# Performance work log

Measured on AMD Instinct MI355X. Metric: run time of the kernel, lower is better.

The kernel has to match this reference:

```python
import jax, jax.numpy as jnp
import numpy as np

NUM_HEADS = 8
DIM_KEY = 64
WINDOW = 16
TEMP = float(np.power(DIM_KEY, 0.5))


def setup_inputs() -> dict:
    key = jax.random.key(0)
    k1, k2, k3, k4 = jax.random.split(key, 4)
    B, T, H = 4, 2048, 512
    std = np.sqrt(2.0 / (H + DIM_KEY))
    return {
        "query": jax.random.normal(k1, (B, T, H), dtype=jnp.float32),
        "key": jax.random.normal(k2, (B, T, H), dtype=jnp.float32),
        "Wq": jax.random.normal(k3, (NUM_HEADS * DIM_KEY, H), dtype=jnp.float32) * std,
        "bq": jnp.zeros((NUM_HEADS * DIM_KEY,), dtype=jnp.float32),
        "Wk": jax.random.normal(k4, (NUM_HEADS * DIM_KEY, H), dtype=jnp.float32) * std,
        "bk": jnp.zeros((NUM_HEADS * DIM_KEY,), dtype=jnp.float32),
    }


def reference(query, key, Wq, bq, Wk, bk):
    B, T, _ = query.shape
    w = WINDOW
    # linear projections, split into heads: [B, T, H, dk]
    q = (jnp.einsum("bti,oi->bto", query, Wq) + bq).reshape(B, T, NUM_HEADS, DIM_KEY)
    k = (jnp.einsum("bti,oi->bto", key, Wk) + bk).reshape(B, T, NUM_HEADS, DIM_KEY)
    # dense scores [B, H, Tq, Tk]
    attn = jnp.einsum("bqhd,bkhd->bhqk", q, k) / TEMP
    # window mask (get_window_mask): allowed where i-w <= j <= i+w
    i = jnp.arange(T)[:, None]
    j = jnp.arange(T)[None, :]
    allowed = (j >= i - w) & (j <= i + w)  # [T, T]
    attn = jnp.where(allowed[None, None], attn, -jnp.inf)
    attn = jax.nn.softmax(attn, axis=-1)
    # select mask gather (get_select_mask): each row keeps 2w+1 cols
    # starting at clip(i - w, 0, T - (2w+1))
    starts = jnp.clip(jnp.arange(T) - w, 0, T - (2 * w + 1))  # [T]
    idx = starts[:, None] + jnp.arange(2 * w + 1)[None, :]  # [T, 2w+1]
    out = jnp.take_along_axis(attn, idx[None, None, :, :], axis=-1)
    return out  # [B, NUM_HEADS, T, 2w+1]
```

## Files before the change

### kernel.cpp

```cpp
#include <hip/hip_runtime.h>
#include <hip/hip_bf16.h>
#include <math.h>

#define TT 2048
#define HH 512
#define NH 8
#define DK 64
#define WIN 16
#define NC 33

typedef __attribute__((ext_vector_type(8))) short bf16x8;
typedef __attribute__((ext_vector_type(4))) float f32x4;

__device__ inline ushort f2bf(float f) {
  uint u = __builtin_bit_cast(uint, f);
  return (ushort)((u + 0x7FFFu + ((u >> 16) & 1u)) >> 16);
}
__device__ inline ushort cvt1(float f) {
  __hip_bfloat16 h = __float2bfloat16(f);
  return __builtin_bit_cast(ushort, h);
}

__global__ __launch_bounds__(256) void cvt_w(
    const float* __restrict__ Wq, const float* __restrict__ Wk,
    ushort* __restrict__ Wqb, ushort* __restrict__ Wkb)
{
  const int id = blockIdx.x * 256 + threadIdx.x;
  const float* src = (id < 32768) ? Wq : Wk;
  ushort* dst = (id < 32768) ? Wqb : Wkb;
  const int off = (id & 32767) * 8;
  float4 x = *(const float4*)(src + off);
  float4 y = *(const float4*)(src + off + 4);
  union { ushort s[8]; uint4 v; } pk;
  pk.s[0]=cvt1(x.x); pk.s[1]=cvt1(x.y); pk.s[2]=cvt1(x.z); pk.s[3]=cvt1(x.w);
  pk.s[4]=cvt1(y.x); pk.s[5]=cvt1(y.y); pk.s[6]=cvt1(y.z); pk.s[7]=cvt1(y.w);
  *(uint4*)(dst + off) = pk.v;
}

#define PBM 128
#define PBN 128
#define PBK 64

__global__ __launch_bounds__(256) void proj_mfma(
    const float* __restrict__ Aq, const float* __restrict__ Ak,
    const ushort* __restrict__ Wqb, const ushort* __restrict__ Wkb,
    const float* __restrict__ bq, const float* __restrict__ bk,
    ushort* __restrict__ Qp, ushort* __restrict__ Kp)
{
  __shared__ ushort As[PBM * PBK];
  __shared__ ushort Ws[PBN * PBK];

  const int z = blockIdx.z;
  const float*  A    = z ? Ak  : Aq;
  const ushort* Wb   = z ? Wkb : Wqb;
  const float*  bias = z ? bk  : bq;
  ushort*       C    = z ? Kp  : Qp;

  const int m0 = blockIdx.x * PBM;
  const int n0 = blockIdx.y * PBN;
  const int t  = threadIdx.x;
  const int l  = t & 63;
  const int w  = t >> 6;
  const int wr = (w >> 1) * 64;
  const int wc = (w & 1) * 64;
  const int lr = l & 15;
  const int lk8 = (l >> 4) * 8;

  f32x4 acc[4][4] = {};

  for (int k0 = 0; k0 < HH; k0 += PBK) {
#pragma unroll
    for (int p = 0; p < 4; ++p) {
      const int u = p * 256 + t;
      const int r = u >> 3, c8 = u & 7;
      const ushort* gsrc = Wb + (size_t)(n0 + r) * HH + k0 + c8 * 8;
      __builtin_amdgcn_global_load_lds(
          (const __attribute__((address_space(1))) uint*)gsrc,
          (__attribute__((address_space(3))) uint*)(Ws + p * 2048 + w * 512),
          16, 0, 0);
    }
#pragma unroll
    for (int p = 0; p < 4; ++p) {
      const int u = p * 256 + t;
      const int r = u >> 3, c8 = u & 7;
      const float* g = A + (size_t)(m0 + r) * HH + k0 + c8 * 8;
      float4 x = ((const float4*)g)[0], y = ((const float4*)g)[1];
      union { ushort s[8]; uint4 v; } pk;
      pk.s[0]=cvt1(x.x); pk.s[1]=cvt1(x.y); pk.s[2]=cvt1(x.z); pk.s[3]=cvt1(x.w);
      pk.s[4]=cvt1(y.x); pk.s[5]=cvt1(y.y); pk.s[6]=cvt1(y.z); pk.s[7]=cvt1(y.w);
      *(uint4*)&As[u * 8] = pk.v;
    }
    __syncthreads();

#pragma unroll
    for (int kk = 0; kk < PBK; kk += 32) {
      bf16x8 af[4], bf[4];
#pragma unroll
      for (int m = 0; m < 4; ++m)
        af[m] = *(const bf16x8*)&As[(wr + m * 16 + lr) * PBK + kk + lk8];
#pragma unroll
      for (int n = 0; n < 4; ++n)
        bf[n] = *(const bf16x8*)&Ws[(wc + n * 16 + lr) * PBK + kk + lk8];
#pragma unroll
      for (int m = 0; m < 4; ++m)
#pragma unroll
        for (int n = 0; n < 4; ++n)
          acc[m][n] = __builtin_amdgcn_mfma_f32_16x16x32_bf16(af[m], bf[n], acc[m][n], 0, 0, 0);
    }
    __syncthreads();
  }

#pragma unroll
  for (int n = 0; n < 4; ++n) {
    const int col = n0 + wc + n * 16 + lr;
    const float bc = bias[col];
#pragma unroll
    for (int m = 0; m < 4; ++m) {
      const int rbase = m0 + wr + m * 16 + (l >> 4) * 4;
#pragma unroll
      for (int q = 0; q < 4; ++q)
        C[(size_t)(rbase + q) * HH + col] = f2bf(acc[m][n][q] + bc);
    }
  }
}

__global__ __launch_bounds__(256) void attn_mfma(
    const ushort* __restrict__ Q, const ushort* __restrict__ Kp,
    float* __restrict__ out)
{
  const int gw = blockIdx.x * 4 + (threadIdx.x >> 6);
  const int h = gw & 7;
  const int tile = gw >> 3;
  const int b = tile >> 7;
  const int i0 = (tile & 127) * 16;
  const int l = threadIdx.x & 63;
  const int lo = l & 15;
  const int hi = l >> 4;

  int jb = i0 - WIN;
  if (jb < 0) jb = 0;
  if (jb > TT - NC) jb = TT - NC;

  const size_t qbase = ((size_t)(b * TT + i0 + lo)) * HH + h * DK + hi * 8;
  bf16x8 aq0 = *(const bf16x8*)(Q + qbase);
  bf16x8 aq1 = *(const bf16x8*)(Q + qbase + 32);

  f32x4 acc[3] = {};
#pragma unroll
  for (int a = 0; a < 3; ++a) {
    int j = jb + a * 16 + lo;
    if (j > TT - 1) j = TT - 1;
    const size_t kbase = ((size_t)(b * TT + j)) * HH + h * DK + hi * 8;
    bf16x8 bk0 = *(const bf16x8*)(Kp + kbase);
    bf16x8 bk1 = *(const bf16x8*)(Kp + kbase + 32);
    acc[a] = __builtin_amdgcn_mfma_f32_16x16x32_bf16(aq0, bk0, acc[a], 0, 0, 0);
    acc[a] = __builtin_amdgcn_mfma_f32_16x16x32_bf16(aq1, bk1, acc[a], 0, 0, 0);
  }

  float e[3][4];
  float inv[4];
#pragma unroll
  for (int q = 0; q < 4; ++q) {
    const int i = i0 + hi * 4 + q;
    float s0, s1, s2;
    {
      const int j0 = jb + lo, j1 = j0 + 16, j2 = j0 + 32;
      s0 = (j0 >= i - WIN && j0 <= i + WIN && j0 < TT) ? acc[0][q] * 0.125f : -INFINITY;
      s1 = (j1 >= i - WIN && j1 <= i + WIN && j1 < TT) ? acc[1][q] * 0.125f : -INFINITY;
      s2 = (j2 >= i - WIN && j2 <= i + WIN && j2 < TT) ? acc[2][q] * 0.125f : -INFINITY;
    }
    float m = fmaxf(fmaxf(s0, s1), s2);
#pragma unroll
    for (int off = 8; off; off >>= 1) m = fmaxf(m, __shfl_xor(m, off));
    const float e0 = __expf(s0 - m);
    const float e1 = __expf(s1 - m);
    const float e2 = __expf(s2 - m);
    e[0][q] = e0; e[1][q] = e1; e[2][q] = e2;
    float sum = e0 + e1 + e2;
#pragma unroll
    for (int off = 8; off; off >>= 1) sum += __shfl_xor(sum, off);
    inv[q] = 1.0f / sum;
  }

  const size_t obase = ((size_t)(b * NH + h)) * TT * NC;
#pragma unroll
  for (int q = 0; q < 4; ++q) {
    const int i = i0 + hi * 4 + q;
    int st = i - WIN;
    if (st < 0) st = 0;
    if (st > TT - NC) st = TT - NC;
#pragma unroll
    for (int a = 0; a < 3; ++a) {
      const int c = jb + a * 16 + lo - st;
      if (c >= 0 && c < NC)
        out[obase + (size_t)i * NC + c] = e[a][q] * inv[q];
    }
  }
}

extern "C" void kernel_launch(void* const* d_in, const int* in_sizes, int n_in,
                              void* d_out, int out_size, void* d_ws, size_t ws_size,
                              hipStream_t stream)
{
  const float* query = (const float*)d_in[0];
  const float* key   = (const float*)d_in[1];
  const float* Wq    = (const float*)d_in[2];
  const float* bq    = (const float*)d_in[3];
  const float* Wk    = (const float*)d_in[4];
  const float* bk    = (const float*)d_in[5];
  float* out = (float*)d_out;

  const int B = 4, M = B * TT;
  ushort* Wqb = (ushort*)d_ws;
  ushort* Wkb = Wqb + (size_t)HH * HH;
  ushort* Qp  = Wkb + (size_t)HH * HH;
  ushort* Kp  = Qp + (size_t)M * HH;

  cvt_w<<<256, 256, 0, stream>>>(Wq, Wk, Wqb, Wkb);
  proj_mfma<<<dim3(M / PBM, HH / PBN, 2), 256, 0, stream>>>(
      query, key, Wqb, Wkb, bq, bk, Qp, Kp);
  attn_mfma<<<dim3((M / 16) * NH / 4), 256, 0, stream>>>(Qp, Kp, out);
}
```

Before: 37.25 us.

## Retile projection GEMM so each block computes all 512 output columns

The projection kernel now uses 64-row tiles covering the full 512-wide output. It runs 512 threads (8 waves, each owning 64 columns) and stages the whole weight K-slice in LDS. The goal is to load and convert each fp32 activation row to bf16 only once instead of once per column tile, which removes redundant activation reads and conversions. In exchange LDS use per block goes up (72KB), the grid shrinks to 256 blocks, and every block re-streams the full weight matrix, which may lower occupancy.

```diff
diff --git a/kernel.cpp b/kernel.cpp
--- a/kernel.cpp
+++ b/kernel.cpp
@@ -37,58 +37,53 @@
   *(uint4*)(dst + off) = pk.v;
 }
 
-#define PBM 128
-#define PBN 128
+#define PBM 64
 #define PBK 64
 
-__global__ __launch_bounds__(256) void proj_mfma(
+__global__ __launch_bounds__(512) void proj_fused(
     const float* __restrict__ Aq, const float* __restrict__ Ak,
     const ushort* __restrict__ Wqb, const ushort* __restrict__ Wkb,
     const float* __restrict__ bq, const float* __restrict__ bk,
     ushort* __restrict__ Qp, ushort* __restrict__ Kp)
 {
   __shared__ ushort As[PBM * PBK];
-  __shared__ ushort Ws[PBN * PBK];
-
-  const int z = blockIdx.z;
+  __shared__ ushort Ws[HH * PBK];
+
+  const int z = blockIdx.y;
   const float*  A    = z ? Ak  : Aq;
   const ushort* Wb   = z ? Wkb : Wqb;
   const float*  bias = z ? bk  : bq;
   ushort*       C    = z ? Kp  : Qp;
 
   const int m0 = blockIdx.x * PBM;
-  const int n0 = blockIdx.y * PBN;
   const int t  = threadIdx.x;
   const int l  = t & 63;
   const int w  = t >> 6;
-  const int wr = (w >> 1) * 64;
-  const int wc = (w & 1) * 64;
   const int lr = l & 15;
-  const int lk8 = (l >> 4) * 8;
+  const int hi = l >> 4;
+  const int lk8 = hi * 8;
 
   f32x4 acc[4][4] = {};
 
   for (int k0 = 0; k0 < HH; k0 += PBK) {
 #pragma unroll
-    for (int p = 0; p < 4; ++p) {
-      const int u = p * 256 + t;
+    for (int p = 0; p < 8; ++p) {
+      const int u = p * 512 + t;
       const int r = u >> 3, c8 = u & 7;
-      const ushort* gsrc = Wb + (size_t)(n0 + r) * HH + k0 + c8 * 8;
       __builtin_amdgcn_global_load_lds(
-          (const __attribute__((address_space(1))) uint*)gsrc,
-          (__attribute__((address_space(3))) uint*)(Ws + p * 2048 + w * 512),
+          (const __attribute__((address_space(1))) uint*)
+              (Wb + (size_t)r * HH + k0 + c8 * 8),
+          (__attribute__((address_space(3))) uint*)(Ws + p * 4096 + w * 512),
           16, 0, 0);
     }
-#pragma unroll
-    for (int p = 0; p < 4; ++p) {
-      const int u = p * 256 + t;
-      const int r = u >> 3, c8 = u & 7;
+    {
+      const int r = t >> 3, c8 = t & 7;
       const float* g = A + (size_t)(m0 + r) * HH + k0 + c8 * 8;
       float4 x = ((const float4*)g)[0], y = ((const float4*)g)[1];
       union { ushort s[8]; uint4 v; } pk;
       pk.s[0]=cvt1(x.x); pk.s[1]=cvt1(x.y); pk.s[2]=cvt1(x.z); pk.s[3]=cvt1(x.w);
       pk.s[4]=cvt1(y.x); pk.s[5]=cvt1(y.y); pk.s[6]=cvt1(y.z); pk.s[7]=cvt1(y.w);
-      *(uint4*)&As[u * 8] = pk.v;
+      *(uint4*)&As[t * 8] = pk.v;
     }
     __syncthreads();
 
@@ -97,10 +92,10 @@
       bf16x8 af[4], bf[4];
 #pragma unroll
       for (int m = 0; m < 4; ++m)
-        af[m] = *(const bf16x8*)&As[(wr + m * 16 + lr) * PBK + kk + lk8];
+        af[m] = *(const bf16x8*)&As[(m * 16 + lr) * PBK + kk + lk8];
 #pragma unroll
       for (int n = 0; n < 4; ++n)
-        bf[n] = *(const bf16x8*)&Ws[(wc + n * 16 + lr) * PBK + kk + lk8];
+        bf[n] = *(const bf16x8*)&Ws[(w * 64 + n * 16 + lr) * PBK + kk + lk8];
 #pragma unroll
       for (int m = 0; m < 4; ++m)
 #pragma unroll
@@ -112,11 +107,11 @@
 
 #pragma unroll
   for (int n = 0; n < 4; ++n) {
-    const int col = n0 + wc + n * 16 + lr;
+    const int col = w * 64 + n * 16 + lr;
     const float bc = bias[col];
 #pragma unroll
     for (int m = 0; m < 4; ++m) {
-      const int rbase = m0 + wr + m * 16 + (l >> 4) * 4;
+      const int rbase = m0 + m * 16 + hi * 4;
 #pragma unroll
       for (int q = 0; q < 4; ++q)
         C[(size_t)(rbase + q) * HH + col] = f2bf(acc[m][n][q] + bc);
@@ -162,13 +157,10 @@
 #pragma unroll
   for (int q = 0; q < 4; ++q) {
     const int i = i0 + hi * 4 + q;
-    float s0, s1, s2;
-    {
-      const int j0 = jb + lo, j1 = j0 + 16, j2 = j0 + 32;
-      s0 = (j0 >= i - WIN && j0 <= i + WIN && j0 < TT) ? acc[0][q] * 0.125f : -INFINITY;
-      s1 = (j1 >= i - WIN && j1 <= i + WIN && j1 < TT) ? acc[1][q] * 0.125f : -INFINITY;
-      s2 = (j2 >= i - WIN && j2 <= i + WIN && j2 < TT) ? acc[2][q] * 0.125f : -INFINITY;
-    }
+    const int j0 = jb + lo, j1 = j0 + 16, j2 = j0 + 32;
+    float s0 = (j0 >= i - WIN && j0 <= i + WIN && j0 < TT) ? acc[0][q] * 0.125f : -INFINITY;
+    float s1 = (j1 >= i - WIN && j1 <= i + WIN && j1 < TT) ? acc[1][q] * 0.125f : -INFINITY;
+    float s2 = (j2 >= i - WIN && j2 <= i + WIN && j2 < TT) ? acc[2][q] * 0.125f : -INFINITY;
     float m = fmaxf(fmaxf(s0, s1), s2);
 #pragma unroll
     for (int off = 8; off; off >>= 1) m = fmaxf(m, __shfl_xor(m, off));
@@ -216,8 +208,8 @@
   ushort* Qp  = Wkb + (size_t)HH * HH;
   ushort* Kp  = Qp + (size_t)M * HH;
 
-  cvt_w<<<256, 256, 0, stream>>>(Wq, Wk, Wqb, Wkb);
-  proj_mfma<<<dim3(M / PBM, HH / PBN, 2), 256, 0, stream>>>(
+  cvt_w<<<dim3(256), 256, 0, stream>>>(Wq, Wk, Wqb, Wkb);
+  proj_fused<<<dim3(M / PBM, 2), 512, 0, stream>>>(
       query, key, Wqb, Wkb, bq, bk, Qp, Kp);
   attn_mfma<<<dim3((M / 16) * NH / 4), 256, 0, stream>>>(Qp, Kp, out);
 }
```

Measured after the change: 43.56 us. +16.9%, slower.
